# Kernel tuning notes

Measured on AMD Instinct MI355X. Metric: run time of the kernel, lower is better.

The kernel has to match this reference:

```python
import jax, jax.numpy as jnp
import numpy as np

NUM_EMBEDDING = 512
EMBEDDING_DIM = 64
COMMITMENT_COST = 0.25


def setup_inputs() -> dict:
    key = jax.random.key(0)
    k1, k2 = jax.random.split(key)
    inputs = jax.random.normal(k1, (32, EMBEDDING_DIM, 64, 64), dtype=jnp.float32)
    # nn.Embedding weight init: uniform(-1/K, 1/K)
    weight = jax.random.uniform(
        k2, (NUM_EMBEDDING, EMBEDDING_DIM), dtype=jnp.float32,
        minval=-1.0 / NUM_EMBEDDING, maxval=1.0 / NUM_EMBEDDING)
    return {"inputs": inputs, "weight": weight}


def reference(inputs, weight):
    B, C, H, W = inputs.shape  # C == EMBEDDING_DIM
    K = weight.shape[0]
    sg = jax.lax.stop_gradient

    # NCHW -> NHWC -> [N, D]
    x = jnp.transpose(inputs, (0, 2, 3, 1)).reshape(-1, C)

    distances = (jnp.sum(x * x, axis=1, keepdims=True)
                 + jnp.sum(weight * weight, axis=1)
                 - 2.0 * jnp.matmul(x, weight.T))
    encoding_indices = jnp.argmin(distances, axis=1)  # [N]

    # one-hot scatter, as in the original
    encodings = jax.nn.one_hot(encoding_indices, K, dtype=x.dtype)  # [N, K]
    # quantized = encodings @ E  (== gather E[idx])
    quantized = jnp.matmul(encodings, weight)  # [N, D]

    q_latent_loss = jnp.mean((sg(quantized) - x) ** 2)
    e_latent_loss = jnp.mean((quantized - sg(x)) ** 2)
    loss = q_latent_loss + COMMITMENT_COST * e_latent_loss

    # straight-through estimator
    quantized_st = x + sg(quantized - x)

    avg_probs = jnp.mean(encodings, axis=0)  # [K]
    perplexity = jnp.exp(-jnp.sum(avg_probs * jnp.log(avg_probs + 1e-10)))

    # [N, D] -> [B, H, W, D] -> [B, D, H, W]
    quantized_out = jnp.transpose(quantized_st.reshape(B, H, W, C), (0, 3, 1, 2))
    return loss, quantized_out, perplexity, encodings
```

## Files before the change

### kernel.cpp

```cpp
#include <hip/hip_runtime.h>

#define BHW 262144
#define OUT_Q_OFF 1
#define OUT_P_OFF 8388609
#define OUT_E_OFF 8388610


typedef __attribute__((ext_vector_type(8))) short short8;
typedef __attribute__((ext_vector_type(4))) float f32x4;
typedef __attribute__((ext_vector_type(2))) float f32x2;

__device__ __forceinline__ unsigned short f2bf(float f) {
    union { float f; unsigned u; } c; c.f = f;
    unsigned r = (c.u + 0x7FFFu + ((c.u >> 16) & 1u)) >> 16;
    return (unsigned short)r;
}

__global__ __launch_bounds__(512) void vq_init(const float* __restrict__ W, float* __restrict__ ws) {
    const int tid = blockIdx.x * 512 + threadIdx.x;
    if (tid < 512) {
        const float4* W4 = (const float4*)W;
        float s = 0.f;
#pragma unroll
        for (int i = 0; i < 16; ++i) {
            float4 v = W4[tid * 16 + i];
            s = fmaf(v.x, v.x, s); s = fmaf(v.y, v.y, s);
            s = fmaf(v.z, v.z, s); s = fmaf(v.w, v.w, s);
        }
        ws[768 + tid] = s;
    } else {
        const int c  = tid - 512;
        const int l  = c & 63;
        const int j  = (c >> 6) & 1;
        const int tn = c >> 7;
        const int n  = tn * 16 + (l & 15);
        const int k0 = j * 32 + ((l >> 4) & 3) * 8;
        const float* src = W + n * 64 + k0;
        unsigned h0 = f2bf(-2.f * src[0]) | ((unsigned)f2bf(-2.f * src[1]) << 16);
        unsigned h1 = f2bf(-2.f * src[2]) | ((unsigned)f2bf(-2.f * src[3]) << 16);
        unsigned h2 = f2bf(-2.f * src[4]) | ((unsigned)f2bf(-2.f * src[5]) << 16);
        unsigned h3 = f2bf(-2.f * src[6]) | ((unsigned)f2bf(-2.f * src[7]) << 16);
        uint4* dst = (uint4*)(ws + 1280);
        dst[c] = make_uint4(h0, h1, h2, h3);
    }
}

__global__ __launch_bounds__(64) void vq_main(const float* __restrict__ X,
                                              const float* __restrict__ W,
                                              float* __restrict__ out,
                                              float* __restrict__ ws) {
    const int l    = threadIdx.x;
    const int nlow = l & 15;
    const int kg   = l >> 4;
    const int rowbase = blockIdx.x * 16;
    const int b  = rowbase >> 12;
    const int h  = (rowbase >> 6) & 63;
    const int w0 = rowbase & 63;

    const float* xr = X + (size_t)b * BHW + (size_t)h * 64 + (w0 + nlow);
    float xf[16];
#pragma unroll
    for (int e = 0; e < 8; ++e) xf[e]     = xr[(size_t)(kg * 8 + e) * 4096];
#pragma unroll
    for (int e = 0; e < 8; ++e) xf[8 + e] = xr[(size_t)(32 + kg * 8 + e) * 4096];
    short8 a0, a1;
#pragma unroll
    for (int e = 0; e < 8; ++e) { a0[e] = (short)f2bf(xf[e]); a1[e] = (short)f2bf(xf[8 + e]); }

    const short8* __restrict__ B8  = (const short8*)(ws + 1280);
    const float*  __restrict__ wsq = ws + 768;
    float bS[4]; int bK[4];
#pragma unroll
    for (int r = 0; r < 4; ++r) { bS[r] = 3.4e38f; bK[r] = 0; }

#pragma unroll 2
    for (int tn = 0; tn < 32; ++tn) {
        short8 f0 = B8[tn * 128 + l];
        short8 f1 = B8[tn * 128 + 64 + l];
        const float wq = wsq[tn * 16 + nlow];
        f32x4 acc = {wq, wq, wq, wq};
        acc = __builtin_amdgcn_mfma_f32_16x16x32_bf16(a0, f0, acc, 0, 0, 0);
        acc = __builtin_amdgcn_mfma_f32_16x16x32_bf16(a1, f1, acc, 0, 0, 0);
        const int n = tn * 16 + nlow;
#pragma unroll
        for (int r = 0; r < 4; ++r) {
            if (acc[r] < bS[r]) { bS[r] = acc[r]; bK[r] = n; }
        }
    }
#pragma unroll
    for (int r = 0; r < 4; ++r) {
#pragma unroll
        for (int mask = 1; mask <= 8; mask <<= 1) {
            float os = __shfl_xor(bS[r], mask);
            int   ok = __shfl_xor(bK[r], mask);
            if (os < bS[r] || (os == bS[r] && ok < bK[r])) { bS[r] = os; bK[r] = ok; }
        }
    }

    int rowBk = 0;
    int myBk  = 0;
    f32x2* encB = (f32x2*)(out + OUT_E_OFF);
    const size_t Rbase = (size_t)rowbase;
#pragma unroll
    for (int m = 0; m < 16; ++m) {
        int bkm = __shfl(bK[m & 3], (m >> 2) * 16);
        if (nlow == m) rowBk = bkm;
        if (l == m)    myBk = bkm;
        f32x2* erow = encB + (Rbase + m) * 256;
#pragma unroll
        for (int c = 0; c < 4; ++c) {
            int p = c * 64 + l;
            f32x2 v;
            v.x = (bkm == 2 * p)     ? 1.f : 0.f;
            v.y = (bkm == 2 * p + 1) ? 1.f : 0.f;
            erow[p] = v;
        }
    }
    if (l < 16) atomicAdd((unsigned*)ws + 256 + myBk, 1u);

    const float4* W4 = (const float4*)W;
    float4 q0 = W4[rowBk * 16 + kg * 2];
    float4 q1 = W4[rowBk * 16 + kg * 2 + 1];
    float4 q2 = W4[rowBk * 16 + 8 + kg * 2];
    float4 q3 = W4[rowBk * 16 + 8 + kg * 2 + 1];
    float qv[16] = {q0.x, q0.y, q0.z, q0.w, q1.x, q1.y, q1.z, q1.w,
                    q2.x, q2.y, q2.z, q2.w, q3.x, q3.y, q3.z, q3.w};
    float lsum = 0.f;
    float* op = out + OUT_Q_OFF + (size_t)b * BHW + (size_t)h * 64 + (w0 + nlow);
#pragma unroll
    for (int e = 0; e < 8; ++e) {
        float d0 = qv[e] - xf[e];
        lsum = fmaf(d0, d0, lsum);
        op[(size_t)(kg * 8 + e) * 4096] = xf[e] + d0;
        float d1 = qv[8 + e] - xf[8 + e];
        lsum = fmaf(d1, d1, lsum);
        op[(size_t)(32 + kg * 8 + e) * 4096] = xf[8 + e] + d1;
    }

#pragma unroll
    for (int off = 32; off >= 1; off >>= 1) lsum += __shfl_down(lsum, off);
    if (l == 0) atomicAdd(ws + (blockIdx.x & 255), lsum);
}

__global__ __launch_bounds__(512) void vq_fin(const float* __restrict__ ws, float* __restrict__ out) {
    __shared__ float redP[8], redL[8];
    const int t = threadIdx.x;
    const unsigned* counts = (const unsigned*)ws + 256;
    float p = (float)counts[t] * (1.0f / 131072.0f);
    float s = p * logf(p + 1e-10f);
    float lp = (t < 256) ? ws[t] : 0.f;
#pragma unroll
    for (int off = 32; off >= 1; off >>= 1) {
        s  += __shfl_down(s, off);
        lp += __shfl_down(lp, off);
    }
    if ((t & 63) == 0) { redP[t >> 6] = s; redL[t >> 6] = lp; }
    __syncthreads();
    if (t == 0) {
        float tp = 0.f, tl = 0.f;
#pragma unroll
        for (int i = 0; i < 8; ++i) { tp += redP[i]; tl += redL[i]; }
        out[OUT_P_OFF] = expf(-tp);
        out[0] = tl * (1.25f / 8388608.0f);
    }
}

extern "C" void kernel_launch(void* const* d_in, const int* in_sizes, int n_in,
                              void* d_out, int out_size, void* d_ws, size_t ws_size,
                              hipStream_t stream) {
    const float* X = (const float*)d_in[0];
    const float* W = (const float*)d_in[1];
    float* out = (float*)d_out;
    float* ws  = (float*)d_ws;

    (void)hipMemsetAsync(d_ws, 0, 768 * sizeof(float), stream);
    vq_init<<<9, 512, 0, stream>>>(W, ws);
    vq_main<<<8192, 64, 0, stream>>>(X, W, out, ws);
    vq_fin<<<1, 512, 0, stream>>>(ws, out);
}
```

Baseline: 116.5 us.

## Split one-hot encoding write into bulk zero-fill plus index scatter kernel

Instead of each wave writing full one-hot rows with per-element compares, odd blocks of a combined kernel zero-fill the entire encodings buffer with 16-byte stores, while even blocks run the VQ search with four waves per block and save argmin indices to the workspace. A separate scatter kernel then writes the 1.0 entries. The aim is wider, more uniform stores for the 512 MB output and better occupancy from larger blocks. The cost is an extra kernel launch, an index round-trip through the workspace, and scattered single-float writes that depend on the zero-fill finishing before the scatter kernel runs.

After: 141.0 us. +20.9%, slower.

```diff
diff --git a/kernel.cpp b/kernel.cpp
--- a/kernel.cpp
+++ b/kernel.cpp
@@ -5,6 +5,7 @@
 #define OUT_P_OFF 8388609
 #define OUT_E_OFF 8388610
 
+#define IDX_W 17664
 
 typedef __attribute__((ext_vector_type(8))) short short8;
 typedef __attribute__((ext_vector_type(4))) float f32x4;
@@ -45,14 +46,36 @@
     }
 }
 
-__global__ __launch_bounds__(64) void vq_main(const float* __restrict__ X,
-                                              const float* __restrict__ W,
-                                              float* __restrict__ out,
-                                              float* __restrict__ ws) {
-    const int l    = threadIdx.x;
+__global__ __launch_bounds__(256) void vq_k1(const float* __restrict__ X,
+                                             const float* __restrict__ W,
+                                             float* __restrict__ out,
+                                             float* __restrict__ ws) {
+    const int t = threadIdx.x;
+
+    if (blockIdx.x & 1) {
+        const int f = blockIdx.x >> 1;
+        f32x4* dst = (f32x4*)(out + OUT_E_OFF + 2);
+        const f32x4 z = {0.f, 0.f, 0.f, 0.f};
+        const int base = f * 8192;
+#pragma unroll
+        for (int i = 0; i < 32; ++i) {
+            int c = base + i * 256 + t;
+            if (c < 16777215) dst[c] = z;
+        }
+        if (f == 0 && t == 0) {
+            f32x2 z2 = {0.f, 0.f};
+            *(f32x2*)(out + OUT_E_OFF) = z2;
+            *(f32x2*)(out + 75497472) = z2;
+        }
+        return;
+    }
+
+    const int l    = t & 63;
+    const int wv   = t >> 6;
     const int nlow = l & 15;
     const int kg   = l >> 4;
-    const int rowbase = blockIdx.x * 16;
+    const int gw   = (blockIdx.x >> 1) * 4 + wv;
+    const int rowbase = gw * 16;
     const int b  = rowbase >> 12;
     const int h  = (rowbase >> 6) & 63;
     const int w0 = rowbase & 63;
@@ -99,24 +122,16 @@
 
     int rowBk = 0;
     int myBk  = 0;
-    f32x2* encB = (f32x2*)(out + OUT_E_OFF);
-    const size_t Rbase = (size_t)rowbase;
 #pragma unroll
     for (int m = 0; m < 16; ++m) {
         int bkm = __shfl(bK[m & 3], (m >> 2) * 16);
         if (nlow == m) rowBk = bkm;
         if (l == m)    myBk = bkm;
-        f32x2* erow = encB + (Rbase + m) * 256;
-#pragma unroll
-        for (int c = 0; c < 4; ++c) {
-            int p = c * 64 + l;
-            f32x2 v;
-            v.x = (bkm == 2 * p)     ? 1.f : 0.f;
-            v.y = (bkm == 2 * p + 1) ? 1.f : 0.f;
-            erow[p] = v;
-        }
-    }
-    if (l < 16) atomicAdd((unsigned*)ws + 256 + myBk, 1u);
+    }
+    if (l < 16) {
+        ((int*)ws)[IDX_W + rowbase + l] = myBk;
+        atomicAdd((unsigned*)ws + 256 + myBk, 1u);
+    }
 
     const float4* W4 = (const float4*)W;
     float4 q0 = W4[rowBk * 16 + kg * 2];
@@ -139,7 +154,14 @@
 
 #pragma unroll
     for (int off = 32; off >= 1; off >>= 1) lsum += __shfl_down(lsum, off);
-    if (l == 0) atomicAdd(ws + (blockIdx.x & 255), lsum);
+    if (l == 0) atomicAdd(ws + (gw & 255), lsum);
+}
+
+__global__ __launch_bounds__(256) void vq_scatter(const float* __restrict__ ws,
+                                                  float* __restrict__ out) {
+    const int row = blockIdx.x * 256 + threadIdx.x;
+    const int bk  = ((const int*)ws)[IDX_W + row];
+    out[OUT_E_OFF + (size_t)row * 512 + bk] = 1.0f;
 }
 
 __global__ __launch_bounds__(512) void vq_fin(const float* __restrict__ ws, float* __restrict__ out) {
@@ -175,6 +197,7 @@
 
     (void)hipMemsetAsync(d_ws, 0, 768 * sizeof(float), stream);
     vq_init<<<9, 512, 0, stream>>>(W, ws);
-    vq_main<<<8192, 64, 0, stream>>>(X, W, out, ws);
+    vq_k1<<<4096, 256, 0, stream>>>(X, W, out, ws);
+    vq_scatter<<<512, 256, 0, stream>>>(ws, out);
     vq_fin<<<1, 512, 0, stream>>>(ws, out);
 }
```

## Split one-hot encoding write into separate aligned 16-byte store kernel

Applied to the files above, without the earlier changes.

The fused kernel now writes only per-row code indices to workspace, and a new kernel expands them into the one-hot encoding matrix using 16-byte aligned stores, handling the 2-float output offset misalignment at row boundaries. This replaces the previous 8-byte strided stores issued from 64-thread blocks, aiming at better write bandwidth on the large encodings output. It adds an extra launch and an index round-trip through memory.

Result: slower. 165.9 us (+42.4%).

```diff
diff --git a/kernel.cpp b/kernel.cpp
--- a/kernel.cpp
+++ b/kernel.cpp
@@ -5,6 +5,7 @@
 #define OUT_P_OFF 8388609
 #define OUT_E_OFF 8388610
 
+#define IDX_W 17664
 
 typedef __attribute__((ext_vector_type(8))) short short8;
 typedef __attribute__((ext_vector_type(4))) float f32x4;
@@ -45,10 +46,10 @@
     }
 }
 
-__global__ __launch_bounds__(64) void vq_main(const float* __restrict__ X,
-                                              const float* __restrict__ W,
-                                              float* __restrict__ out,
-                                              float* __restrict__ ws) {
+__global__ __launch_bounds__(64) void vq_score(const float* __restrict__ X,
+                                               const float* __restrict__ W,
+                                               float* __restrict__ out,
+                                               float* __restrict__ ws) {
     const int l    = threadIdx.x;
     const int nlow = l & 15;
     const int kg   = l >> 4;
@@ -99,24 +100,16 @@
 
     int rowBk = 0;
     int myBk  = 0;
-    f32x2* encB = (f32x2*)(out + OUT_E_OFF);
-    const size_t Rbase = (size_t)rowbase;
 #pragma unroll
     for (int m = 0; m < 16; ++m) {
         int bkm = __shfl(bK[m & 3], (m >> 2) * 16);
         if (nlow == m) rowBk = bkm;
         if (l == m)    myBk = bkm;
-        f32x2* erow = encB + (Rbase + m) * 256;
-#pragma unroll
-        for (int c = 0; c < 4; ++c) {
-            int p = c * 64 + l;
-            f32x2 v;
-            v.x = (bkm == 2 * p)     ? 1.f : 0.f;
-            v.y = (bkm == 2 * p + 1) ? 1.f : 0.f;
-            erow[p] = v;
-        }
-    }
-    if (l < 16) atomicAdd((unsigned*)ws + 256 + myBk, 1u);
+    }
+    if (l < 16) {
+        ((int*)ws)[IDX_W + rowbase + l] = myBk;
+        atomicAdd((unsigned*)ws + 256 + myBk, 1u);
+    }
 
     const float4* W4 = (const float4*)W;
     float4 q0 = W4[rowBk * 16 + kg * 2];
@@ -142,6 +135,46 @@
     if (l == 0) atomicAdd(ws + (blockIdx.x & 255), lsum);
 }
 
+__global__ __launch_bounds__(256) void vq_enc(const float* __restrict__ ws,
+                                              float* __restrict__ out) {
+    const int t = threadIdx.x;
+    const int* __restrict__ idx = (const int*)ws + IDX_W;
+    f32x4* __restrict__ dst = (f32x4*)(out + OUT_E_OFF + 2);
+    const int base = blockIdx.x * 8192;
+#pragma unroll 4
+    for (int i = 0; i < 32; ++i) {
+        int c = base + i * 256 + t;
+        if (c < 16777215) {
+            int g   = c * 4 + 2;
+            int row = g >> 9;
+            int col = g & 511;
+            int k   = idx[row];
+            f32x4 v;
+            if (col == 510) {
+                int k2 = idx[row + 1];
+                v.x = (k  == 510) ? 1.f : 0.f;
+                v.y = (k  == 511) ? 1.f : 0.f;
+                v.z = (k2 == 0)   ? 1.f : 0.f;
+                v.w = (k2 == 1)   ? 1.f : 0.f;
+            } else {
+                v.x = (col     == k) ? 1.f : 0.f;
+                v.y = (col + 1 == k) ? 1.f : 0.f;
+                v.z = (col + 2 == k) ? 1.f : 0.f;
+                v.w = (col + 3 == k) ? 1.f : 0.f;
+            }
+            dst[c] = v;
+        }
+    }
+    if (blockIdx.x == 0 && t == 0) {
+        int k0 = idx[0];
+        f32x2 hd; hd.x = (k0 == 0) ? 1.f : 0.f; hd.y = (k0 == 1) ? 1.f : 0.f;
+        *(f32x2*)(out + OUT_E_OFF) = hd;
+        int kl = idx[131071];
+        f32x2 tl; tl.x = (kl == 510) ? 1.f : 0.f; tl.y = (kl == 511) ? 1.f : 0.f;
+        *(f32x2*)(out + OUT_E_OFF + (size_t)131071 * 512 + 510) = tl;
+    }
+}
+
 __global__ __launch_bounds__(512) void vq_fin(const float* __restrict__ ws, float* __restrict__ out) {
     __shared__ float redP[8], redL[8];
     const int t = threadIdx.x;
@@ -175,6 +208,7 @@
 
     (void)hipMemsetAsync(d_ws, 0, 768 * sizeof(float), stream);
     vq_init<<<9, 512, 0, stream>>>(W, ws);
-    vq_main<<<8192, 64, 0, stream>>>(X, W, out, ws);
+    vq_score<<<8192, 64, 0, stream>>>(X, W, out, ws);
+    vq_enc<<<2048, 256, 0, stream>>>(ws, out);
     vq_fin<<<1, 512, 0, stream>>>(ws, out);
 }
```

## Stage bf16 codebook in shared memory shared by four waves per block

Applied to the files above, without the earlier changes.

The main kernel now runs 256-thread blocks of four waves, each wave handling 16 rows. The bf16 codebook B-fragments are cooperatively copied from the workspace into LDS in two 32 KB halves, and all waves read them from there instead of each wave streaming them from global/L2. This cuts redundant codebook traffic per row, at the cost of two block-wide barriers per half and 32 KB of LDS per block, which may limit occupancy.

Result: faster. 111.3 us (-4.5%).

```diff
diff --git a/kernel.cpp b/kernel.cpp
--- a/kernel.cpp
+++ b/kernel.cpp
@@ -45,19 +45,23 @@
     }
 }
 
-__global__ __launch_bounds__(64) void vq_main(const float* __restrict__ X,
-                                              const float* __restrict__ W,
-                                              float* __restrict__ out,
-                                              float* __restrict__ ws) {
-    const int l    = threadIdx.x;
+__global__ __launch_bounds__(256) void vq_main(const float* __restrict__ X,
+                                               const float* __restrict__ W,
+                                               float* __restrict__ out,
+                                               float* __restrict__ ws) {
+    const int t    = threadIdx.x;
+    const int l    = t & 63;
+    const int wv   = t >> 6;
     const int nlow = l & 15;
     const int kg   = l >> 4;
-    const int rowbase = blockIdx.x * 16;
-    const int b  = rowbase >> 12;
-    const int h  = (rowbase >> 6) & 63;
-    const int w0 = rowbase & 63;
+    const int rowbase = blockIdx.x * 64;
+    const int b = rowbase >> 12;
+    const int h = (rowbase >> 6) & 63;
+    const int myrow = wv * 16 + nlow;
 
-    const float* xr = X + (size_t)b * BHW + (size_t)h * 64 + (w0 + nlow);
+    __shared__ short8 Btab[2048];
+
+    const float* xr = X + (size_t)b * BHW + (size_t)h * 64 + myrow;
     float xf[16];
 #pragma unroll
     for (int e = 0; e < 8; ++e) xf[e]     = xr[(size_t)(kg * 8 + e) * 4096];
@@ -67,24 +71,32 @@
 #pragma unroll
     for (int e = 0; e < 8; ++e) { a0[e] = (short)f2bf(xf[e]); a1[e] = (short)f2bf(xf[8 + e]); }
 
-    const short8* __restrict__ B8  = (const short8*)(ws + 1280);
-    const float*  __restrict__ wsq = ws + 768;
+    const uint4* __restrict__ gtab = (const uint4*)(ws + 1280);
+    const float* __restrict__ wsq  = ws + 768;
     float bS[4]; int bK[4];
 #pragma unroll
     for (int r = 0; r < 4; ++r) { bS[r] = 3.4e38f; bK[r] = 0; }
 
-#pragma unroll 2
-    for (int tn = 0; tn < 32; ++tn) {
-        short8 f0 = B8[tn * 128 + l];
-        short8 f1 = B8[tn * 128 + 64 + l];
-        const float wq = wsq[tn * 16 + nlow];
-        f32x4 acc = {wq, wq, wq, wq};
-        acc = __builtin_amdgcn_mfma_f32_16x16x32_bf16(a0, f0, acc, 0, 0, 0);
-        acc = __builtin_amdgcn_mfma_f32_16x16x32_bf16(a1, f1, acc, 0, 0, 0);
-        const int n = tn * 16 + nlow;
+    for (int half = 0; half < 2; ++half) {
+        __syncthreads();
+        uint4* bt = (uint4*)Btab;
 #pragma unroll
-        for (int r = 0; r < 4; ++r) {
-            if (acc[r] < bS[r]) { bS[r] = acc[r]; bK[r] = n; }
+        for (int i = 0; i < 8; ++i)
+            bt[i * 256 + t] = gtab[half * 2048 + i * 256 + t];
+        __syncthreads();
+#pragma unroll 4
+        for (int tn = 0; tn < 16; ++tn) {
+            short8 f0 = Btab[tn * 128 + l];
+            short8 f1 = Btab[tn * 128 + 64 + l];
+            const int   n  = (half * 16 + tn) * 16 + nlow;
+            const float wq = wsq[n];
+            f32x4 acc = {wq, wq, wq, wq};
+            acc = __builtin_amdgcn_mfma_f32_16x16x32_bf16(a0, f0, acc, 0, 0, 0);
+            acc = __builtin_amdgcn_mfma_f32_16x16x32_bf16(a1, f1, acc, 0, 0, 0);
+#pragma unroll
+            for (int r = 0; r < 4; ++r) {
+                if (acc[r] < bS[r]) { bS[r] = acc[r]; bK[r] = n; }
+            }
         }
     }
 #pragma unroll
@@ -100,7 +112,7 @@
     int rowBk = 0;
     int myBk  = 0;
     f32x2* encB = (f32x2*)(out + OUT_E_OFF);
-    const size_t Rbase = (size_t)rowbase;
+    const size_t Rbase = (size_t)(rowbase + wv * 16);
 #pragma unroll
     for (int m = 0; m < 16; ++m) {
         int bkm = __shfl(bK[m & 3], (m >> 2) * 16);
@@ -126,7 +138,7 @@
     float qv[16] = {q0.x, q0.y, q0.z, q0.w, q1.x, q1.y, q1.z, q1.w,
                     q2.x, q2.y, q2.z, q2.w, q3.x, q3.y, q3.z, q3.w};
     float lsum = 0.f;
-    float* op = out + OUT_Q_OFF + (size_t)b * BHW + (size_t)h * 64 + (w0 + nlow);
+    float* op = out + OUT_Q_OFF + (size_t)b * BHW + (size_t)h * 64 + myrow;
 #pragma unroll
     for (int e = 0; e < 8; ++e) {
         float d0 = qv[e] - xf[e];
@@ -139,7 +151,7 @@
 
 #pragma unroll
     for (int off = 32; off >= 1; off >>= 1) lsum += __shfl_down(lsum, off);
-    if (l == 0) atomicAdd(ws + (blockIdx.x & 255), lsum);
+    if (l == 0) atomicAdd(ws + ((blockIdx.x * 4 + wv) & 255), lsum);
 }
 
 __global__ __launch_bounds__(512) void vq_fin(const float* __restrict__ ws, float* __restrict__ out) {
@@ -175,6 +187,6 @@
 
     (void)hipMemsetAsync(d_ws, 0, 768 * sizeof(float), stream);
     vq_init<<<9, 512, 0, stream>>>(W, ws);
-    vq_main<<<8192, 64, 0, stream>>>(X, W, out, ws);
+    vq_main<<<2048, 256, 0, stream>>>(X, W, out, ws);
     vq_fin<<<1, 512, 0, stream>>>(ws, out);
 }
```
